# Optimization experiments

Measured on AMD Instinct MI355X. Metric: run time of the kernel, lower is better.

## Reference

```python
import jax, jax.numpy as jnp
import numpy as np

G, N, E = 4, 50000, 400000   # subgraphs, nodes/graph, edges/graph
D = 128                      # num_node_feat = num_g_hid = out_g_ch
L = 3                        # num_layers
NE, AH = 8, 64               # num_expert, num_att_hid
FE = 8                       # num_edge_feat (unused by GIN conv)
LN_EPS = 1e-5


def setup_inputs() -> dict:
    key = jax.random.key(0)
    ks = jax.random.split(key, 12)
    s = 1.0 / np.sqrt(D)
    inp = {
        "decomp_x": jax.random.normal(ks[0], (G, N, D), dtype=jnp.float32),
        "decomp_edge_index": jax.random.randint(ks[1], (G, 2, E), 0, N, dtype=jnp.int32),
        "decomp_edge_attr": jax.random.normal(ks[2], (G, E, FE), dtype=jnp.float32),
        # GIN MLP params per layer: Linear(D,D) -> ReLU -> Linear(D,D), stored [in,out]
        "Ws1": jax.random.uniform(ks[3], (L, D, D), jnp.float32, -s, s),
        "bs1": jax.random.uniform(ks[4], (L, D), jnp.float32, -s, s),
        "Ws2": jax.random.uniform(ks[5], (L, D, D), jnp.float32, -s, s),
        "bs2": jax.random.uniform(ks[6], (L, D), jnp.float32, -s, s),
        "ln_g": jnp.ones((L, D), jnp.float32),
        "ln_b": jnp.zeros((L, D), jnp.float32),
        # Attention: w1 [n_hidden, v_hidden], w2 [n_expert, n_hidden]
        "att_w1": jax.random.uniform(ks[7], (AH, D), jnp.float32, -1.0 / np.sqrt(D), 1.0 / np.sqrt(D)),
        "att_w2": jax.random.uniform(ks[8], (NE, AH), jnp.float32, -1.0 / np.sqrt(AH), 1.0 / np.sqrt(AH)),
    }
    return inp


def _layer_norm(h, g, b):
    mu = jnp.mean(h, axis=-1, keepdims=True)
    var = jnp.var(h, axis=-1, keepdims=True)
    return (h - mu) * jax.lax.rsqrt(var + LN_EPS) * g + b


def _gin_graph(x, edge_index, Ws1, bs1, Ws2, bs2, ln_g, ln_b):
    # x: [N, D]; edge_index: [2, E] (src, dst)
    src, dst = edge_index[0], edge_index[1]
    for l in range(L):
        identity = x
        # GINConv (eps=0): MLP(x_i + sum_{j->i} x_j)
        agg = jax.ops.segment_sum(x[src], dst, num_segments=N)  # gather+scatter
        h = x + agg
        h = jnp.maximum(h @ Ws1[l] + bs1[l], 0.0) @ Ws2[l] + bs2[l]
        if l < L - 1:
            h = h + identity  # same dims, no projection
        x = _layer_norm(h, ln_g[l], ln_b[l])
    return jnp.sum(x, axis=0)  # [D] graph readout (sum over nodes)


def reference(decomp_x, decomp_edge_index, decomp_edge_attr,
              Ws1, bs1, Ws2, bs2, ln_g, ln_b, att_w1, att_w2):
    # edge_attr is unused by the GIN conv path (only NaN-checked in torch)
    g = jax.vmap(_gin_graph, in_axes=(0, 0, None, None, None, None, None, None))(
        decomp_x, decomp_edge_index, Ws1, bs1, Ws2, bs2, ln_g, ln_b)  # [G, D]
    # Attention pooling over subgraph vectors
    support = jnp.tanh(att_w1 @ g.T)                 # [AH, G]
    att = jax.nn.softmax(att_w2 @ support, axis=1)   # [NE, G]
    pooled = att @ g                                 # [NE, D]
    return pooled.reshape(1, NE * D)                 # [1, NE*D]
```

## Files before the change

### kernel.cpp

```cpp
#include <hip/hip_runtime.h>
#include <math.h>

#define G 4
#define NN 50000
#define EE 400000
#define D 128
#define LN_EPS 1e-5f
#define BPG 782

typedef _Float16 f16;
typedef _Float16 f16x4 __attribute__((ext_vector_type(4)));
typedef _Float16 f16x8 __attribute__((ext_vector_type(8)));
typedef float f32x4 __attribute__((ext_vector_type(4)));


__global__ __launch_bounds__(256) void hist_kernel(const int* __restrict__ ei, int* __restrict__ deg) {
    int idx = blockIdx.x * 256 + threadIdx.x;
    if (idx >= G * EE) return;
    int g = idx / EE, e = idx - g * EE;
    int dst = ei[g * 2 * EE + EE + e];
    atomicAdd(&deg[g * NN + dst], 1);
}

__global__ __launch_bounds__(1024) void scan_kernel(const int* __restrict__ deg, int* __restrict__ row_start,
                                                    int* __restrict__ cursor) {
    int g = blockIdx.x, t = threadIdx.x;
    const int C = (NN + 1023) / 1024;
    __shared__ int sums[1024];
    int start = t * C, end = min(start + C, NN);
    int s = 0;
    for (int i = start; i < end; ++i) s += deg[g * NN + i];
    sums[t] = s;
    __syncthreads();
    for (int off = 1; off < 1024; off <<= 1) {
        int v = (t >= off) ? sums[t - off] : 0;
        __syncthreads();
        sums[t] += v;
        __syncthreads();
    }
    int run = (t == 0) ? 0 : sums[t - 1];
    for (int i = start; i < end; ++i) {
        row_start[g * (NN + 1) + i] = run;
        cursor[g * NN + i] = run;
        run += deg[g * NN + i];
    }
    if (t == 1023) row_start[g * (NN + 1) + NN] = sums[1023];
}

__global__ __launch_bounds__(256) void place_kernel(const int* __restrict__ ei, int* __restrict__ cursor,
                                                    int* __restrict__ csr_src) {
    int idx = blockIdx.x * 256 + threadIdx.x;
    if (idx >= G * EE) return;
    int g = idx / EE, e = idx - g * EE;
    int src = ei[g * 2 * EE + e];
    int dst = ei[g * 2 * EE + EE + e];
    int pos = atomicAdd(&cursor[g * NN + dst], 1);
    csr_src[g * EE + pos] = src;
}


__global__ __launch_bounds__(256) void cast_x_kernel(const float* __restrict__ x, f16* __restrict__ o) {
    int i = blockIdx.x * 256 + threadIdx.x;
    float4 v = ((const float4*)x)[i];
    f16x4 h = {(f16)v.x, (f16)v.y, (f16)v.z, (f16)v.w};
    ((f16x4*)o)[i] = h;
}

__global__ __launch_bounds__(256) void cast_w_kernel(const float* __restrict__ Ws1, const float* __restrict__ Ws2,
                                                     f16* __restrict__ Wt) {
    int e = blockIdx.x * 256 + threadIdx.x;
    int mat = e >> 14, r = (e >> 7) & 127, c = e & 127;
    const float* src = (mat < 3) ? (Ws1 + mat * 16384) : (Ws2 + (mat - 3) * 16384);
    Wt[e] = (f16)src[c * 128 + r];
}


__global__ __launch_bounds__(256, 4) void gin_layer(
    const f16* __restrict__ Xin, f16* __restrict__ Xout,
    const int* __restrict__ row_start, const int* __restrict__ csr_src,
    const f16* __restrict__ W1t, const f16* __restrict__ W2t,
    const float* __restrict__ b1, const float* __restrict__ b2,
    const float* __restrict__ lng, const float* __restrict__ lnb,
    int has_res, int do_read, float* __restrict__ gvec)
{
    __shared__ f16 A[64][136];
    __shared__ f16 ID[64][136];
    __shared__ float colsum[128];

    int t = threadIdx.x;
    int g = blockIdx.x / BPG, bb = blockIdx.x - g * BPG;
    int nrow0 = bb * 64;
    long row0 = (long)g * NN + nrow0;
    int valid = min(64, NN - nrow0);

    if (do_read) {
        if (t < 128) colsum[t] = 0.f;
        __syncthreads();
    }

    {
        int grp = t >> 4, lane = t & 15;
        const int* rs = row_start + g * (NN + 1);
        const int* srcs = csr_src + (long)g * EE;
        long gbase = (long)g * NN * 16;
        const f16x8* Xv = (const f16x8*)Xin;
#pragma unroll
        for (int i = 0; i < 4; ++i) {
            int r = grp * 4 + i;
            if (r < valid) {
                int n = nrow0 + r;
                f16x8 self = Xv[(row0 + r) * 16 + lane];
                if (has_res) *(f16x8*)&ID[r][lane * 8] = self;
                float acc[8];
#pragma unroll
                for (int j = 0; j < 8; ++j) acc[j] = (float)self[j];
                int s0 = rs[n], s1 = rs[n + 1];
                int k = s0;
                for (; k + 3 < s1; k += 4) {
                    f16x8 v0 = Xv[gbase + (long)srcs[k] * 16 + lane];
                    f16x8 v1 = Xv[gbase + (long)srcs[k + 1] * 16 + lane];
                    f16x8 v2 = Xv[gbase + (long)srcs[k + 2] * 16 + lane];
                    f16x8 v3 = Xv[gbase + (long)srcs[k + 3] * 16 + lane];
#pragma unroll
                    for (int j = 0; j < 8; ++j)
                        acc[j] += ((float)v0[j] + (float)v1[j]) + ((float)v2[j] + (float)v3[j]);
                }
                for (; k < s1; ++k) {
                    f16x8 v0 = Xv[gbase + (long)srcs[k] * 16 + lane];
#pragma unroll
                    for (int j = 0; j < 8; ++j) acc[j] += (float)v0[j];
                }
                f16x8 o;
#pragma unroll
                for (int j = 0; j < 8; ++j) o[j] = (f16)acc[j];
                *(f16x8*)&A[r][lane * 8] = o;
            } else {
                f16x8 z = {0, 0, 0, 0, 0, 0, 0, 0};
                *(f16x8*)&A[r][lane * 8] = z;
            }
        }
    }

    int w = t >> 6, l = t & 63, q = l >> 4, cl = l & 15;
    int mrow = w * 16 + cl;

    const f16x8* Wb1 = (const f16x8*)W1t + (cl * 16 + q);
    f32x4 acc[8];
#pragma unroll
    for (int ns = 0; ns < 8; ++ns) acc[ns] = (f32x4){0.f, 0.f, 0.f, 0.f};
#pragma unroll
    for (int kc = 0; kc < 4; ++kc) {
        f16x8 a = *(const f16x8*)&A[mrow][kc * 32 + q * 8];
#pragma unroll
        for (int ns = 0; ns < 8; ++ns) {
            f16x8 b = Wb1[ns * 256 + kc * 4];
            acc[ns] = __builtin_amdgcn_mfma_f32_16x16x32_f16(a, b, acc[ns], 0, 0, 0);
        }
    }

#pragma unroll
    for (int ns = 0; ns < 8; ++ns) {
        float bv = b1[ns * 16 + cl];
#pragma unroll
        for (int r = 0; r < 4; ++r) {
            float v = fmaxf(acc[ns][r] + bv, 0.f);
            A[w * 16 + q * 4 + r][ns * 16 + cl] = (f16)v;
        }
    }

    const f16x8* Wb2 = (const f16x8*)W2t + (cl * 16 + q);
    f32x4 acc2[8];
#pragma unroll
    for (int ns = 0; ns < 8; ++ns) acc2[ns] = (f32x4){0.f, 0.f, 0.f, 0.f};
#pragma unroll
    for (int kc = 0; kc < 4; ++kc) {
        f16x8 a = *(const f16x8*)&A[mrow][kc * 32 + q * 8];
#pragma unroll
        for (int ns = 0; ns < 8; ++ns) {
            f16x8 b = Wb2[ns * 256 + kc * 4];
            acc2[ns] = __builtin_amdgcn_mfma_f32_16x16x32_f16(a, b, acc2[ns], 0, 0, 0);
        }
    }

    float o[8][4];
    float gm[8], gb[8];
#pragma unroll
    for (int ns = 0; ns < 8; ++ns) {
        int col = ns * 16 + cl;
        float b2v = b2[col];
        gm[ns] = lng[col];
        gb[ns] = lnb[col];
#pragma unroll
        for (int r = 0; r < 4; ++r) o[ns][r] = acc2[ns][r] + b2v;
    }
    if (has_res) {
#pragma unroll
        for (int r = 0; r < 4; ++r) {
            int lr = w * 16 + q * 4 + r;
#pragma unroll
            for (int ns = 0; ns < 8; ++ns) o[ns][r] += (float)ID[lr][ns * 16 + cl];
        }
    }

#pragma unroll
    for (int r = 0; r < 4; ++r) {
        float s1 = 0.f, s2 = 0.f;
#pragma unroll
        for (int ns = 0; ns < 8; ++ns) { s1 += o[ns][r]; s2 += o[ns][r] * o[ns][r]; }
        s1 += __shfl_xor(s1, 1); s2 += __shfl_xor(s2, 1);
        s1 += __shfl_xor(s1, 2); s2 += __shfl_xor(s2, 2);
        s1 += __shfl_xor(s1, 4); s2 += __shfl_xor(s2, 4);
        s1 += __shfl_xor(s1, 8); s2 += __shfl_xor(s2, 8);
        float mean = s1 * (1.f / 128.f);
        float var = s2 * (1.f / 128.f) - mean * mean;
        float rstd = rsqrtf(var + LN_EPS);
#pragma unroll
        for (int ns = 0; ns < 8; ++ns) o[ns][r] = (o[ns][r] - mean) * rstd * gm[ns] + gb[ns];
    }

    if (!do_read) {
#pragma unroll
        for (int ns = 0; ns < 8; ++ns)
#pragma unroll
            for (int r = 0; r < 4; ++r)
                A[w * 16 + q * 4 + r][ns * 16 + cl] = (f16)o[ns][r];
        int rr = w * 16 + (l >> 2), seg = l & 3;
        if (rr < valid) {
            f16* dst = Xout + (row0 + rr) * 128 + seg * 32;
            const f16* srcp = &A[rr][seg * 32];
            *(f16x8*)(dst)      = *(const f16x8*)(srcp);
            *(f16x8*)(dst + 8)  = *(const f16x8*)(srcp + 8);
            *(f16x8*)(dst + 16) = *(const f16x8*)(srcp + 16);
            *(f16x8*)(dst + 24) = *(const f16x8*)(srcp + 24);
        }
    } else {
#pragma unroll
        for (int ns = 0; ns < 8; ++ns) {
            float v = 0.f;
#pragma unroll
            for (int r = 0; r < 4; ++r) {
                int lr = w * 16 + q * 4 + r;
                if (lr < valid) v += o[ns][r];
            }
            v += __shfl_xor(v, 16);
            v += __shfl_xor(v, 32);
            if (l < 16) atomicAdd(&colsum[ns * 16 + cl], v);
        }
        __syncthreads();
        if (t < 128) atomicAdd(&gvec[g * 128 + t], colsum[t]);
    }
}


__global__ __launch_bounds__(256) void att_kernel(const float* __restrict__ gvec, const float* __restrict__ w1,
                                                  const float* __restrict__ w2, float* __restrict__ out) {
    __shared__ float sup[64][4];
    __shared__ float att[8][4];
    int t = threadIdx.x;
    int ah = t >> 2, gg = t & 3;
    float d = 0.f;
    for (int k = 0; k < 128; ++k) d += w1[ah * 128 + k] * gvec[gg * 128 + k];
    sup[ah][gg] = tanhf(d);
    __syncthreads();
    if (t < 32) {
        int ne = t >> 2, g2 = t & 3;
        float sc = 0.f;
        for (int k = 0; k < 64; ++k) sc += w2[ne * 64 + k] * sup[k][g2];
        att[ne][g2] = sc;
    }
    __syncthreads();
    if (t < 8) {
        float m = fmaxf(fmaxf(att[t][0], att[t][1]), fmaxf(att[t][2], att[t][3]));
        float e0 = expf(att[t][0] - m), e1 = expf(att[t][1] - m);
        float e2 = expf(att[t][2] - m), e3 = expf(att[t][3] - m);
        float inv = 1.f / (e0 + e1 + e2 + e3);
        att[t][0] = e0 * inv; att[t][1] = e1 * inv; att[t][2] = e2 * inv; att[t][3] = e3 * inv;
    }
    __syncthreads();
    for (int o = t; o < 1024; o += 256) {
        int ne = o >> 7, dd = o & 127;
        float v = 0.f;
        for (int g2 = 0; g2 < 4; ++g2) v += att[ne][g2] * gvec[g2 * 128 + dd];
        out[o] = v;
    }
}


extern "C" void kernel_launch(void* const* d_in, const int* in_sizes, int n_in,
                              void* d_out, int out_size, void* d_ws, size_t ws_size,
                              hipStream_t stream) {
    const float* x   = (const float*)d_in[0];
    const int*   ei  = (const int*)d_in[1];
    const float* Ws1 = (const float*)d_in[3];
    const float* bs1 = (const float*)d_in[4];
    const float* Ws2 = (const float*)d_in[5];
    const float* bs2 = (const float*)d_in[6];
    const float* lng = (const float*)d_in[7];
    const float* lnb = (const float*)d_in[8];
    const float* aw1 = (const float*)d_in[9];
    const float* aw2 = (const float*)d_in[10];

    char* ws = (char*)d_ws;
    f16*   XA       = (f16*)(ws);
    f16*   XB       = (f16*)(ws + 51200000);
    int*   csr_src  = (int*)(ws + 102400000);
    int*   row_start= (int*)(ws + 108800000);
    int*   cursor   = (int*)(ws + 109600256);
    int*   deg      = (int*)(ws + 110400256);
    f16*   Wt       = (f16*)(ws + 111200256);
    float* gvec     = (float*)(ws + 111396864);

    hipMemsetAsync(deg, 0, G * NN * sizeof(int), stream);
    hipMemsetAsync(gvec, 0, G * D * sizeof(float), stream);

    hist_kernel<<<(G * EE + 255) / 256, 256, 0, stream>>>(ei, deg);
    scan_kernel<<<G, 1024, 0, stream>>>(deg, row_start, cursor);
    place_kernel<<<(G * EE + 255) / 256, 256, 0, stream>>>(ei, cursor, csr_src);

    cast_x_kernel<<<(G * NN * D / 4) / 256, 256, 0, stream>>>(x, XA);
    cast_w_kernel<<<(6 * D * D) / 256, 256, 0, stream>>>(Ws1, Ws2, Wt);

    f16* Xcur = XA;
    f16* Xnxt = XB;
    for (int l = 0; l < 3; ++l) {
        gin_layer<<<G * BPG, 256, 0, stream>>>(Xcur, Xnxt, row_start, csr_src,
                                               Wt + l * D * D, Wt + (3 + l) * D * D,
                                               bs1 + l * D, bs2 + l * D,
                                               lng + l * D, lnb + l * D,
                                               (l < 2) ? 1 : 0, (l == 2) ? 1 : 0, gvec);
        f16* tmp = Xcur; Xcur = Xnxt; Xnxt = tmp;
    }
    att_kernel<<<1, 256, 0, stream>>>(gvec, aw1, aw2, (float*)d_out);
}
```

Baseline: 981.2 us.

## Bucket CSR neighbors by source range and interleave block-to-graph mapping

The CSR build now splits each node's neighbor list into four buckets by source-node range. The gather phase walks all rows of a block bucket by bucket, so concurrent loads hit a narrower slice of the feature table and should get better L2/MALL locality. Block indices are also remapped so adjacent blocks cover different graphs and row halves. This adds a larger degree array and scan, a more complex gather loop with more register state, and a smaller unroll depth.

```diff
diff --git a/kernel.cpp b/kernel.cpp
--- a/kernel.cpp
+++ b/kernel.cpp
@@ -7,6 +7,10 @@
 #define D 128
 #define LN_EPS 1e-5f
 #define BPG 782
+#define NB 4
+#define BSZ 12500
+#define M (NN * NB)
+#define SM 200008
 
 typedef _Float16 f16;
 typedef _Float16 f16x4 __attribute__((ext_vector_type(4)));
@@ -18,18 +22,19 @@
     int idx = blockIdx.x * 256 + threadIdx.x;
     if (idx >= G * EE) return;
     int g = idx / EE, e = idx - g * EE;
+    int src = ei[g * 2 * EE + e];
     int dst = ei[g * 2 * EE + EE + e];
-    atomicAdd(&deg[g * NN + dst], 1);
-}
-
-__global__ __launch_bounds__(1024) void scan_kernel(const int* __restrict__ deg, int* __restrict__ row_start,
-                                                    int* __restrict__ cursor) {
+    int b = src / BSZ;
+    atomicAdd(&deg[g * M + dst * NB + b], 1);
+}
+
+__global__ __launch_bounds__(1024) void scan_kernel(const int* __restrict__ deg, int* __restrict__ E) {
     int g = blockIdx.x, t = threadIdx.x;
-    const int C = (NN + 1023) / 1024;
+    const int C = (M + 1023) / 1024;
     __shared__ int sums[1024];
-    int start = t * C, end = min(start + C, NN);
+    int start = t * C, end = min(start + C, M);
     int s = 0;
-    for (int i = start; i < end; ++i) s += deg[g * NN + i];
+    for (int i = start; i < end; ++i) s += deg[g * M + i];
     sums[t] = s;
     __syncthreads();
     for (int off = 1; off < 1024; off <<= 1) {
@@ -39,22 +44,23 @@
         __syncthreads();
     }
     int run = (t == 0) ? 0 : sums[t - 1];
+    int* Eg = E + g * SM;
+    if (t == 0) Eg[0] = 0;
     for (int i = start; i < end; ++i) {
-        row_start[g * (NN + 1) + i] = run;
-        cursor[g * NN + i] = run;
-        run += deg[g * NN + i];
-    }
-    if (t == 1023) row_start[g * (NN + 1) + NN] = sums[1023];
-}
-
-__global__ __launch_bounds__(256) void place_kernel(const int* __restrict__ ei, int* __restrict__ cursor,
+        Eg[1 + i] = run;
+        run += deg[g * M + i];
+    }
+}
+
+__global__ __launch_bounds__(256) void place_kernel(const int* __restrict__ ei, int* __restrict__ E,
                                                     int* __restrict__ csr_src) {
     int idx = blockIdx.x * 256 + threadIdx.x;
     if (idx >= G * EE) return;
     int g = idx / EE, e = idx - g * EE;
     int src = ei[g * 2 * EE + e];
     int dst = ei[g * 2 * EE + EE + e];
-    int pos = atomicAdd(&cursor[g * NN + dst], 1);
+    int b = src / BSZ;
+    int pos = atomicAdd(&E[g * SM + 1 + dst * NB + b], 1);
     csr_src[g * EE + pos] = src;
 }
 
@@ -77,7 +83,7 @@
 
 __global__ __launch_bounds__(256, 4) void gin_layer(
     const f16* __restrict__ Xin, f16* __restrict__ Xout,
-    const int* __restrict__ row_start, const int* __restrict__ csr_src,
+    const int* __restrict__ E, const int* __restrict__ csr_src,
     const f16* __restrict__ W1t, const f16* __restrict__ W2t,
     const float* __restrict__ b1, const float* __restrict__ b2,
     const float* __restrict__ lng, const float* __restrict__ lnb,
@@ -88,7 +94,10 @@
     __shared__ float colsum[128];
 
     int t = threadIdx.x;
-    int g = blockIdx.x / BPG, bb = blockIdx.x - g * BPG;
+    int slot = blockIdx.x & 7;
+    int gi = blockIdx.x >> 3;
+    int g = slot & 3;
+    int bb = (slot >> 2) * 391 + gi;
     int nrow0 = bb * 64;
     long row0 = (long)g * NN + nrow0;
     int valid = min(64, NN - nrow0);
@@ -100,10 +109,13 @@
 
     {
         int grp = t >> 4, lane = t & 15;
-        const int* rs = row_start + g * (NN + 1);
+        const int* Eg = E + g * SM;
         const int* srcs = csr_src + (long)g * EE;
         long gbase = (long)g * NN * 16;
         const f16x8* Xv = (const f16x8*)Xin;
+
+        float acc[4][8];
+        int bnd[4][5];
 #pragma unroll
         for (int i = 0; i < 4; ++i) {
             int r = grp * 4 + i;
@@ -111,33 +123,46 @@
                 int n = nrow0 + r;
                 f16x8 self = Xv[(row0 + r) * 16 + lane];
                 if (has_res) *(f16x8*)&ID[r][lane * 8] = self;
-                float acc[8];
-#pragma unroll
-                for (int j = 0; j < 8; ++j) acc[j] = (float)self[j];
-                int s0 = rs[n], s1 = rs[n + 1];
+#pragma unroll
+                for (int j = 0; j < 8; ++j) acc[i][j] = (float)self[j];
+                int4 b4 = *(const int4*)&Eg[n * NB];
+                bnd[i][0] = b4.x; bnd[i][1] = b4.y; bnd[i][2] = b4.z; bnd[i][3] = b4.w;
+                bnd[i][4] = Eg[n * NB + 4];
+            } else {
+#pragma unroll
+                for (int j = 0; j < 8; ++j) acc[i][j] = 0.f;
+#pragma unroll
+                for (int j = 0; j < 5; ++j) bnd[i][j] = 0;
+            }
+        }
+
+#pragma unroll
+        for (int b = 0; b < NB; ++b) {
+#pragma unroll
+            for (int i = 0; i < 4; ++i) {
+                int s0 = bnd[i][b], s1 = bnd[i][b + 1];
                 int k = s0;
-                for (; k + 3 < s1; k += 4) {
+                for (; k + 1 < s1; k += 2) {
                     f16x8 v0 = Xv[gbase + (long)srcs[k] * 16 + lane];
                     f16x8 v1 = Xv[gbase + (long)srcs[k + 1] * 16 + lane];
-                    f16x8 v2 = Xv[gbase + (long)srcs[k + 2] * 16 + lane];
-                    f16x8 v3 = Xv[gbase + (long)srcs[k + 3] * 16 + lane];
-#pragma unroll
-                    for (int j = 0; j < 8; ++j)
-                        acc[j] += ((float)v0[j] + (float)v1[j]) + ((float)v2[j] + (float)v3[j]);
+#pragma unroll
+                    for (int j = 0; j < 8; ++j) acc[i][j] += (float)v0[j] + (float)v1[j];
                 }
-                for (; k < s1; ++k) {
+                if (k < s1) {
                     f16x8 v0 = Xv[gbase + (long)srcs[k] * 16 + lane];
 #pragma unroll
-                    for (int j = 0; j < 8; ++j) acc[j] += (float)v0[j];
+                    for (int j = 0; j < 8; ++j) acc[i][j] += (float)v0[j];
                 }
-                f16x8 o;
-#pragma unroll
-                for (int j = 0; j < 8; ++j) o[j] = (f16)acc[j];
-                *(f16x8*)&A[r][lane * 8] = o;
-            } else {
-                f16x8 z = {0, 0, 0, 0, 0, 0, 0, 0};
-                *(f16x8*)&A[r][lane * 8] = z;
             }
+        }
+
+#pragma unroll
+        for (int i = 0; i < 4; ++i) {
+            int r = grp * 4 + i;
+            f16x8 o;
+#pragma unroll
+            for (int j = 0; j < 8; ++j) o[j] = (f16)acc[i][j];
+            *(f16x8*)&A[r][lane * 8] = o;
         }
     }
 
@@ -304,18 +329,17 @@
     f16*   XA       = (f16*)(ws);
     f16*   XB       = (f16*)(ws + 51200000);
     int*   csr_src  = (int*)(ws + 102400000);
-    int*   row_start= (int*)(ws + 108800000);
-    int*   cursor   = (int*)(ws + 109600256);
-    int*   deg      = (int*)(ws + 110400256);
-    f16*   Wt       = (f16*)(ws + 111200256);
-    float* gvec     = (float*)(ws + 111396864);
-
-    hipMemsetAsync(deg, 0, G * NN * sizeof(int), stream);
+    int*   E        = (int*)(ws + 108800000);
+    f16*   Wt       = (f16*)(ws + 112000256);
+    float* gvec     = (float*)(ws + 112196864);
+    int*   deg      = (int*)(ws + 51200000);
+
+    hipMemsetAsync(deg, 0, G * M * sizeof(int), stream);
     hipMemsetAsync(gvec, 0, G * D * sizeof(float), stream);
 
     hist_kernel<<<(G * EE + 255) / 256, 256, 0, stream>>>(ei, deg);
-    scan_kernel<<<G, 1024, 0, stream>>>(deg, row_start, cursor);
-    place_kernel<<<(G * EE + 255) / 256, 256, 0, stream>>>(ei, cursor, csr_src);
+    scan_kernel<<<G, 1024, 0, stream>>>(deg, E);
+    place_kernel<<<(G * EE + 255) / 256, 256, 0, stream>>>(ei, E, csr_src);
 
     cast_x_kernel<<<(G * NN * D / 4) / 256, 256, 0, stream>>>(x, XA);
     cast_w_kernel<<<(6 * D * D) / 256, 256, 0, stream>>>(Ws1, Ws2, Wt);
@@ -323,7 +347,7 @@
     f16* Xcur = XA;
     f16* Xnxt = XB;
     for (int l = 0; l < 3; ++l) {
-        gin_layer<<<G * BPG, 256, 0, stream>>>(Xcur, Xnxt, row_start, csr_src,
+        gin_layer<<<G * BPG, 256, 0, stream>>>(Xcur, Xnxt, E, csr_src,
                                                Wt + l * D * D, Wt + (3 + l) * D * D,
                                                bs1 + l * D, bs2 + l * D,
                                                lng + l * D, lnb + l * D,
```

Result: slower. 1.279 ms (+30.4%).
